# Optimization experiments

Hardware: AMD Instinct MI355X
Metric: run time of the kernel (lower is better)

## Reference

```python
import jax, jax.numpy as jnp
import numpy as np

B = 2; R_PER = 512; R = B * R_PER; RM_PER = 128; RM = B * RM_PER
NUM_CLASSES = 81; C = 256
IMG_H = 800.0; IMG_W = 800.0
SCALES = (0.25, 0.125, 0.0625, 0.03125)  # FPN strides 4,8,16,32
REG_W = (10.0, 10.0, 5.0, 5.0)
LOG_1000_16 = 4.135166556742356  # math.log(1000/16)


def _prep(c, size):
    # torchvision roi_align (aligned=False) coordinate handling
    valid = (c > -1.0) & (c < size)
    c = jnp.clip(c, 0.0, size - 1.0)
    lo = jnp.clip(jnp.floor(c), 0.0, size - 2.0).astype(jnp.int32)
    frac = c - lo.astype(c.dtype)
    return lo, frac, valid


def roi_align(feat, boxes, b_idx, scale, out_size, sr=2):
    # feat [B,C,H,W], boxes [R,4] in image coords, b_idx [R] int
    _, Cn, H, W = feat.shape
    bb = boxes * scale
    x1, y1 = bb[:, 0], bb[:, 1]
    rw = jnp.maximum(bb[:, 2] - x1, 1.0)
    rh = jnp.maximum(bb[:, 3] - y1, 1.0)
    n = out_size * sr
    g = (jnp.arange(n, dtype=feat.dtype) + 0.5) / (sr * out_size)
    ys = y1[:, None] + rh[:, None] * g[None, :]  # [R,n]
    xs = x1[:, None] + rw[:, None] * g[None, :]
    y0, ly, yv = _prep(ys, H)
    x0, lx, xv = _prep(xs, W)
    bi = b_idx[:, None, None]
    yy = y0[:, :, None]; xx = x0[:, None, :]
    f00 = feat[bi, :, yy, xx]          # [R,n,n,C]
    f01 = feat[bi, :, yy, xx + 1]
    f10 = feat[bi, :, yy + 1, xx]
    f11 = feat[bi, :, yy + 1, xx + 1]
    ly_ = ly[:, :, None, None]; lx_ = lx[:, None, :, None]
    v = (f00 * (1 - ly_) * (1 - lx_) + f01 * (1 - ly_) * lx_
         + f10 * ly_ * (1 - lx_) + f11 * ly_ * lx_)
    mask = (yv[:, :, None] & xv[:, None, :]).astype(v.dtype)[..., None]
    v = v * mask
    Rn = boxes.shape[0]
    v = v.reshape(Rn, out_size, sr, out_size, sr, Cn).mean(axis=(2, 4))
    return jnp.transpose(v, (0, 3, 1, 2))  # [R,C,out,out]


def multiscale_roi_align(feats, boxes, b_idx, out_size):
    area = jnp.maximum(boxes[:, 2] - boxes[:, 0], 0.0) * jnp.maximum(boxes[:, 3] - boxes[:, 1], 0.0)
    lvl = jnp.clip(jnp.floor(4.0 + jnp.log2(jnp.sqrt(area) / 224.0 + 1e-6)), 2.0, 5.0).astype(jnp.int32) - 2
    out = 0.0
    for i, (f, s) in enumerate(zip(feats, SCALES)):
        out = out + roi_align(f, boxes, b_idx, s, out_size) * (lvl == i)[:, None, None, None].astype(f.dtype)
    return out


def decode_boxes(deltas, boxes):
    # deltas [R,K,4], boxes [R,4]
    wx, wy, ww, wh = REG_W
    w = boxes[:, 2] - boxes[:, 0]; h = boxes[:, 3] - boxes[:, 1]
    cx = boxes[:, 0] + 0.5 * w; cy = boxes[:, 1] + 0.5 * h
    dx = deltas[..., 0] / wx; dy = deltas[..., 1] / wy
    dw = jnp.minimum(deltas[..., 2] / ww, LOG_1000_16)
    dh = jnp.minimum(deltas[..., 3] / wh, LOG_1000_16)
    pcx = dx * w[:, None] + cx[:, None]; pcy = dy * h[:, None] + cy[:, None]
    pw = jnp.exp(dw) * w[:, None]; ph = jnp.exp(dh) * h[:, None]
    out = jnp.stack([pcx - 0.5 * pw, pcy - 0.5 * ph, pcx + 0.5 * pw, pcy + 0.5 * ph], axis=-1)
    hi = jnp.array([IMG_W, IMG_H, IMG_W, IMG_H], dtype=out.dtype)
    return jnp.clip(out, 0.0, hi)  # process_box clip-to-image


def conv3x3(x, w, b):
    y = jax.lax.conv_general_dilated(x, w, (1, 1), ((1, 1), (1, 1)),
                                     dimension_numbers=('NCHW', 'OIHW', 'NCHW'))
    return jax.nn.relu(y + b[None, :, None, None])


def _forward(feat0, feat1, feat2, feat3, proposals, fc1_w, fc1_b, fc2_w, fc2_b,
             cls_w, cls_b, bbox_w, bbox_b, mconv_w, mconv_b, deconv_w, deconv_b,
             mlogit_w, mlogit_b, batch_idx):
    feats = (feat0, feat1, feat2, feat3)
    # box branch
    bf = multiscale_roi_align(feats, proposals, batch_idx, 7).reshape(R, -1)  # [R, 256*49]
    x = jax.nn.relu(bf @ fc1_w.T + fc1_b)
    x = jax.nn.relu(x @ fc2_w.T + fc2_b)
    scores = jax.nn.softmax(x @ cls_w.T + cls_b, axis=-1)          # [R,81]
    deltas = (x @ bbox_w.T + bbox_b).reshape(R, NUM_CLASSES, 4)
    boxes = decode_boxes(deltas, proposals)                        # [R,81,4]
    # mask branch on top-of-list detections (RM_PER per image), box at argmax fg class
    idx_m = jnp.concatenate([jnp.arange(RM_PER), R_PER + jnp.arange(RM_PER)])
    labels = jnp.argmax(scores[idx_m, 1:], axis=-1) + 1            # [RM]
    mboxes = boxes[idx_m, labels]                                  # [RM,4]
    mf = multiscale_roi_align(feats, mboxes, batch_idx[idx_m], 14)  # [RM,256,14,14]
    for i in range(4):
        mf = conv3x3(mf, mconv_w[i], mconv_b[i])
    # ConvTranspose2d k=2 s=2 (non-overlapping) as einsum, PyTorch IOHW weights
    t = jnp.einsum('bcij,copq->boipjq', mf, deconv_w).reshape(RM, C, 28, 28)
    t = jax.nn.relu(t + deconv_b[None, :, None, None])
    ml = jnp.einsum('bchw,oc->bohw', t, mlogit_w) + mlogit_b[None, :, None, None]
    masks = jax.nn.sigmoid(ml[jnp.arange(RM), labels])             # [RM,28,28]
    return scores, boxes, masks


def setup_inputs() -> dict:
    key = jax.random.key(0)
    ks = jax.random.split(key, 16)
    rn = lambda i, shape, s=1.0: jax.random.normal(ks[i], shape, dtype=jnp.float32) * s
    feat0 = rn(0, (B, C, 200, 200))
    feat1 = rn(1, (B, C, 100, 100))
    feat2 = rn(2, (B, C, 50, 50))
    feat3 = rn(3, (B, C, 25, 25))
    u = jax.random.uniform(ks[4], (R, 4), dtype=jnp.float32)
    x1 = u[:, 0] * (IMG_W - 64.0); y1 = u[:, 1] * (IMG_H - 64.0)
    w = 16.0 + u[:, 2] * 300.0; h = 16.0 + u[:, 3] * 300.0
    proposals = jnp.stack([x1, y1, jnp.minimum(x1 + w, IMG_W), jnp.minimum(y1 + h, IMG_H)], axis=1)
    batch_idx = jnp.repeat(jnp.arange(B, dtype=jnp.int32), R_PER)
    return dict(
        feat0=feat0, feat1=feat1, feat2=feat2, feat3=feat3,
        proposals=proposals,
        fc1_w=rn(5, (1024, C * 49), 0.01), fc1_b=jnp.zeros(1024, jnp.float32),
        fc2_w=rn(6, (1024, 1024), 0.02), fc2_b=jnp.zeros(1024, jnp.float32),
        cls_w=rn(7, (NUM_CLASSES, 1024), 0.02), cls_b=jnp.zeros(NUM_CLASSES, jnp.float32),
        bbox_w=rn(8, (NUM_CLASSES * 4, 1024), 0.01), bbox_b=jnp.zeros(NUM_CLASSES * 4, jnp.float32),
        mconv_w=rn(9, (4, C, C, 3, 3), 0.03), mconv_b=jnp.zeros((4, C), jnp.float32),
        deconv_w=rn(10, (C, C, 2, 2), 0.06), deconv_b=jnp.zeros(C, jnp.float32),
        mlogit_w=rn(11, (NUM_CLASSES, C), 0.06), mlogit_b=jnp.zeros(NUM_CLASSES, jnp.float32),
        batch_idx=batch_idx,
    )


def reference(feat0, feat1, feat2, feat3, proposals, fc1_w, fc1_b, fc2_w, fc2_b,
              cls_w, cls_b, bbox_w, bbox_b, mconv_w, mconv_b, deconv_w, deconv_b,
              mlogit_w, mlogit_b, batch_idx):
    return _forward(feat0, feat1, feat2, feat3, proposals, fc1_w, fc1_b, fc2_w, fc2_b,
                    cls_w, cls_b, bbox_w, bbox_b, mconv_w, mconv_b, deconv_w, deconv_b,
                    mlogit_w, mlogit_b, batch_idx)
```

## Files before the change

### kernel.cpp

```cpp
#include <hip/hip_runtime.h>


#define NUM_CLASSES 81
#define CDIM 256
#define RTOT 1024
#define RMASK 256
#define LOG1000_16 4.135166556742356f

typedef _Float16 half8v __attribute__((ext_vector_type(8)));
typedef _Float16 half4v __attribute__((ext_vector_type(4)));
typedef float    float4v __attribute__((ext_vector_type(4)));
typedef float    float2a4 __attribute__((ext_vector_type(2), aligned(4)));

__device__ __forceinline__ void gload_lds16(const void* g, void* l) {
    __builtin_amdgcn_global_load_lds(
        (const __attribute__((address_space(1))) void*)g,
        (__attribute__((address_space(3))) void*)l, 16, 0, 0);
}

__global__ __launch_bounds__(256) void transpose_nhwc_kernel(
    const float* __restrict__ in, float* __restrict__ out, int H, int W)
{
    __shared__ float tile[64][65];
    int t = threadIdx.x;
    int xl = t & 63, cq = t >> 6;
    int x0 = blockIdx.x * 64;
    int y  = blockIdx.y;
    int b  = blockIdx.z >> 2;
    int c0 = (blockIdx.z & 3) * 64;

    const float* ip = in + (((size_t)(b*CDIM + c0))*H + y)*W + x0;
    if (x0 + xl < W) {
        #pragma unroll
        for (int i = 0; i < 16; ++i) {
            int cl = cq + i*4;
            tile[cl][xl] = ip[(size_t)cl*H*W + xl];
        }
    }
    __syncthreads();
    float* op = out + (((size_t)b*H + y)*W + x0)*CDIM + c0;
    #pragma unroll
    for (int i = 0; i < 16; ++i) {
        int xw = cq + i*4;
        if (x0 + xw < W)
            op[(size_t)xw*CDIM + xl] = tile[xl][xw];
    }
}

__device__ __forceinline__ void axis_taps(
    float start, float ext, int o, float invn, int N,
    float* wgt, int* idx)
{
    #pragma unroll
    for (int s = 0; s < 2; ++s) {
        int i = o*2 + s;
        float g = ((float)i + 0.5f) * invn;
        float c = start + ext*g;
        float mv = ((c > -1.f) && (c < (float)N)) ? 1.f : 0.f;
        float cl = fminf(fmaxf(c, 0.f), (float)(N-1));
        int   i0 = (int)fminf(floorf(cl), (float)(N-2));
        float l  = cl - (float)i0;
        wgt[s*2+0] = (1.f-l)*mv;
        wgt[s*2+1] = l*mv;
        idx[s*2+0] = i0;
        idx[s*2+1] = i0+1;
    }
}

__global__ __launch_bounds__(256) void roi_align7_nhwc_kernel(
    const float* __restrict__ fT0, const float* __restrict__ fT1,
    const float* __restrict__ fT2, const float* __restrict__ fT3,
    const float* __restrict__ props, const int* __restrict__ bidx,
    _Float16* __restrict__ bf_h, _Float16* __restrict__ bf_l)
{
    __shared__ _Float16 lh[256*49];
    __shared__ _Float16 ll[256*49];
    int r = blockIdx.x, t = threadIdx.x;
    int lane = t & 63, wv = t >> 6;

    float x1 = props[r*4+0], y1 = props[r*4+1];
    float x2 = props[r*4+2], y2 = props[r*4+3];
    float area = fmaxf(x2-x1, 0.f) * fmaxf(y2-y1, 0.f);
    float lf = floorf(4.f + log2f(sqrtf(area)/224.f + 1e-6f));
    lf = fminf(fmaxf(lf, 2.f), 5.f);
    int lvl = (int)lf - 2;

    const float* fT; int H, W; float scale;
    if (lvl == 0)      { fT = fT0; H = 200; W = 200; scale = 0.25f; }
    else if (lvl == 1) { fT = fT1; H = 100; W = 100; scale = 0.125f; }
    else if (lvl == 2) { fT = fT2; H = 50;  W = 50;  scale = 0.0625f; }
    else               { fT = fT3; H = 25;  W = 25;  scale = 0.03125f; }
    int b = bidx[r];
    const float* fb = fT + ((size_t)b*H*W)*CDIM + lane*4;

    float x1s = x1*scale, y1s = y1*scale;
    float rw = fmaxf(x2*scale - x1s, 1.f);
    float rh = fmaxf(y2*scale - y1s, 1.f);

    for (int p = wv; p < 49; p += 4) {
        int oy = p / 7, ox = p % 7;
        float uy[4]; int yr[4];
        axis_taps(y1s, rh, oy, 1.f/14.f, H, uy, yr);
        float wx[4]; int xc[4];
        axis_taps(x1s, rw, ox, 1.f/14.f, W, wx, xc);

        float a0 = 0.f, a1 = 0.f, a2 = 0.f, a3 = 0.f;
        #pragma unroll
        for (int a = 0; a < 4; ++a) {
            const float* rowp = fb + (size_t)(yr[a]*W)*CDIM;
            #pragma unroll
            for (int c2 = 0; c2 < 4; ++c2) {
                float w = uy[a]*wx[c2];
                float4v v = *(const float4v*)(rowp + xc[c2]*CDIM);
                a0 += w*v[0]; a1 += w*v[1]; a2 += w*v[2]; a3 += w*v[3];
            }
        }
        float av[4] = {a0, a1, a2, a3};
        #pragma unroll
        for (int e = 0; e < 4; ++e) {
            float vv = av[e]*0.25f;
            _Float16 h = (_Float16)vv;
            int c = lane*4 + e;
            lh[c*49 + p] = h;
            ll[c*49 + p] = (_Float16)((vv - (float)h)*2048.f);
        }
    }
    __syncthreads();
    size_t ob = (size_t)r*12544;
    for (int k = t; k < 12544; k += 256) {
        bf_h[ob + k] = lh[k];
        bf_l[ob + k] = ll[k];
    }
}

__global__ __launch_bounds__(256) void roi_align14_nhwc_kernel(
    const float* __restrict__ fT0, const float* __restrict__ fT1,
    const float* __restrict__ fT2, const float* __restrict__ fT3,
    const float* __restrict__ mboxes, const int* __restrict__ bidx,
    _Float16* __restrict__ outT)
{
    int mi = blockIdx.x, py = blockIdx.y;
    int t = threadIdx.x;
    int lane = t & 63, wv = t >> 6;

    float x1 = mboxes[mi*4+0], y1 = mboxes[mi*4+1];
    float x2 = mboxes[mi*4+2], y2 = mboxes[mi*4+3];
    float area = fmaxf(x2-x1, 0.f) * fmaxf(y2-y1, 0.f);
    float lf = floorf(4.f + log2f(sqrtf(area)/224.f + 1e-6f));
    lf = fminf(fmaxf(lf, 2.f), 5.f);
    int lvl = (int)lf - 2;

    const float* fT; int H, W; float scale;
    if (lvl == 0)      { fT = fT0; H = 200; W = 200; scale = 0.25f; }
    else if (lvl == 1) { fT = fT1; H = 100; W = 100; scale = 0.125f; }
    else if (lvl == 2) { fT = fT2; H = 50;  W = 50;  scale = 0.0625f; }
    else               { fT = fT3; H = 25;  W = 25;  scale = 0.03125f; }
    int ridx = (mi < 128) ? mi : mi + 384;
    int b = bidx[ridx];
    const float* fb = fT + ((size_t)b*H*W)*CDIM + lane*4;

    float x1s = x1*scale, y1s = y1*scale;
    float rw = fmaxf(x2*scale - x1s, 1.f);
    float rh = fmaxf(y2*scale - y1s, 1.f);

    for (int pp = wv; pp < 49; pp += 4) {
        int p = py*49 + pp;
        int oy = p / 14, ox = p % 14;
        float uy[4]; int yr[4];
        axis_taps(y1s, rh, oy, 1.f/28.f, H, uy, yr);
        float wx[4]; int xc[4];
        axis_taps(x1s, rw, ox, 1.f/28.f, W, wx, xc);

        float a0 = 0.f, a1 = 0.f, a2 = 0.f, a3 = 0.f;
        #pragma unroll
        for (int a = 0; a < 4; ++a) {
            const float* rowp = fb + (size_t)(yr[a]*W)*CDIM;
            #pragma unroll
            for (int c2 = 0; c2 < 4; ++c2) {
                float w = uy[a]*wx[c2];
                float4v v = *(const float4v*)(rowp + xc[c2]*CDIM);
                a0 += w*v[0]; a1 += w*v[1]; a2 += w*v[2]; a3 += w*v[3];
            }
        }
        half4v hv;
        hv[0] = (_Float16)(a0*0.25f);
        hv[1] = (_Float16)(a1*0.25f);
        hv[2] = (_Float16)(a2*0.25f);
        hv[3] = (_Float16)(a3*0.25f);
        *(half4v*)(outT + ((size_t)mi*196 + p)*CDIM + lane*4) = hv;
    }
}

__global__ __launch_bounds__(256) void roi_align7_kernel(
    const float* __restrict__ f0, const float* __restrict__ f1,
    const float* __restrict__ f2, const float* __restrict__ f3,
    const float* __restrict__ props, const int* __restrict__ bidx,
    _Float16* __restrict__ bf_h, _Float16* __restrict__ bf_l)
{
    int r  = blockIdx.x;
    int cg = blockIdx.y;
    int t = threadIdx.x;
    if (t >= 196) return;
    int p  = t % 49;
    int cl = t / 49;
    int oy = p / 7, ox = p % 7;

    float x1 = props[r*4+0], y1 = props[r*4+1];
    float x2 = props[r*4+2], y2 = props[r*4+3];
    float area = fmaxf(x2-x1, 0.f) * fmaxf(y2-y1, 0.f);
    float lf = floorf(4.f + log2f(sqrtf(area)/224.f + 1e-6f));
    lf = fminf(fmaxf(lf, 2.f), 5.f);
    int lvl = (int)lf - 2;

    const float* feat; int H, W; float scale;
    if (lvl == 0)      { feat = f0; H = 200; W = 200; scale = 0.25f; }
    else if (lvl == 1) { feat = f1; H = 100; W = 100; scale = 0.125f; }
    else if (lvl == 2) { feat = f2; H = 50;  W = 50;  scale = 0.0625f; }
    else               { feat = f3; H = 25;  W = 25;  scale = 0.03125f; }
    int b = bidx[r];

    float x1s = x1*scale, y1s = y1*scale;
    float rw = fmaxf(x2*scale - x1s, 1.f);
    float rh = fmaxf(y2*scale - y1s, 1.f);

    int   offs[4];
    float w00[4], w01[4], w10[4], w11[4];
    #pragma unroll
    for (int sy = 0; sy < 2; ++sy) {
        int iy = oy*2 + sy;
        float gy = ((float)iy + 0.5f) / 14.f;
        float yc = y1s + rh*gy;
        bool  yv = (yc > -1.f) && (yc < (float)H);
        float ycl = fminf(fmaxf(yc, 0.f), (float)(H-1));
        int   y0  = (int)fminf(floorf(ycl), (float)(H-2));
        float ly  = ycl - (float)y0;
        #pragma unroll
        for (int sx = 0; sx < 2; ++sx) {
            int ix = ox*2 + sx;
            float gx = ((float)ix + 0.5f) / 14.f;
            float xc = x1s + rw*gx;
            bool  xv = (xc > -1.f) && (xc < (float)W);
            float xcl = fminf(fmaxf(xc, 0.f), (float)(W-1));
            int   x0  = (int)fminf(floorf(xcl), (float)(W-2));
            float lx  = xcl - (float)x0;
            float m = (yv && xv) ? 1.f : 0.f;
            int s = sy*2 + sx;
            offs[s] = y0*W + x0;
            w00[s] = (1.f-ly)*(1.f-lx)*m;
            w01[s] = (1.f-ly)*lx*m;
            w10[s] = ly*(1.f-lx)*m;
            w11[s] = ly*lx*m;
        }
    }

    size_t HW = (size_t)H * W;
    #pragma unroll 4
    for (int k = 0; k < 16; ++k) {
        int c = cg*64 + cl + k*4;
        const float* fb = feat + ((size_t)b*CDIM + c) * HW;
        float acc = 0.f;
        #pragma unroll
        for (int s = 0; s < 4; ++s) {
            const float* q = fb + offs[s];
            float2a4 u = *(const float2a4*)q;
            float2a4 v = *(const float2a4*)(q + W);
            acc += w00[s]*u.x + w01[s]*u.y + w10[s]*v.x + w11[s]*v.y;
        }
        float v = acc * 0.25f;
        _Float16 h = (_Float16)v;
        size_t o = (size_t)r*12544 + c*49 + p;
        bf_h[o] = h;
        bf_l[o] = (_Float16)((v - (float)h) * 2048.f);
    }
}

template<int BMODE>
__global__ __launch_bounds__(512, 2) void gemm_fc2(
    const _Float16* __restrict__ Ah, const _Float16* __restrict__ Al,
    const float* __restrict__ B32,
    const _Float16* __restrict__ Bh16, const _Float16* __restrict__ Bl16,
    float* __restrict__ Cp, int K, int KS, int NS)
{
    __shared__ __align__(16) char smem[2*32768];

    int t = threadIdx.x;
    int lane = t & 63, wave = t >> 6;
    int wm = wave >> 2, wn = wave & 3;
    int ln = lane & 15, q = lane >> 4;

    int gx = gridDim.x, gy = gridDim.y;
    int lin = blockIdx.x + gx*(blockIdx.y + gy*blockIdx.z);
    int per = (gx*gy*(int)gridDim.z) >> 3;
    int nl  = (lin & 7)*per + (lin >> 3);
    int bn  = nl % gx;
    int tmp = nl / gx;
    int bm  = tmp % gy;
    int kz  = tmp / gy;

    size_t kbase = (size_t)kz * KS;
    int arow = t >> 2;
    int achk = (lane & 3) ^ ((lane >> 3) & 3);
    const _Float16* Agh = Ah + (size_t)(bm*128 + arow)*K + kbase + achk*8;
    const _Float16* Agl = Al + (size_t)(bm*128 + arow)*K + kbase + achk*8;
    int adst = wave * 512;

    const _Float16 *Bgh = nullptr, *Bgl = nullptr;
    const float *Bg0 = nullptr, *Bg1 = nullptr;
    int bfdst0 = 0, bfdst1 = 0;
    if constexpr (BMODE == 1) {
        Bgh = Bh16 + (size_t)(bn*128 + arow)*K + kbase + achk*8;
        Bgl = Bl16 + (size_t)(bn*128 + arow)*K + kbase + achk*8;
    } else {
        int brow = t >> 3;
        int bchk = (lane & 7) ^ ((lane >> 3) & 7);
        Bg0 = B32 + (size_t)(bn*128 + brow)*K + kbase + bchk*4;
        Bg1 = Bg0 + (size_t)64*K;
        bfdst0 = wave*256;
        bfdst1 = 2048 + wave*256;
    }

    auto AhB = [&](int b){ return (_Float16*)(smem + b*32768); };
    auto AlB = [&](int b){ return (_Float16*)(smem + b*32768 + 8192); };
    auto BhB = [&](int b){ return (_Float16*)(smem + b*32768 + 16384); };
    auto BlB = [&](int b){ return (_Float16*)(smem + b*32768 + 24576); };
    auto BfB = [&](int b){ return (float*)   (smem + b*32768 + 16384); };

    auto dma = [&](int k0, int b) {
        gload_lds16(Agh + k0, AhB(b) + adst);
        gload_lds16(Agl + k0, AlB(b) + adst);
        if constexpr (BMODE == 1) {
            gload_lds16(Bgh + k0, BhB(b) + adst);
            gload_lds16(Bgl + k0, BlB(b) + adst);
        } else {
            gload_lds16(Bg0 + k0, BfB(b) + bfdst0);
            gload_lds16(Bg1 + k0, BfB(b) + bfdst1);
        }
    };

    float4v acc1[4][2], acc2[4][2];
    #pragma unroll
    for (int i = 0; i < 4; ++i)
        #pragma unroll
        for (int j = 0; j < 2; ++j) {
            acc1[i][j] = (float4v){0.f,0.f,0.f,0.f};
            acc2[i][j] = (float4v){0.f,0.f,0.f,0.f};
        }

    int cq = (q ^ ((ln >> 1) & 3)) * 8;

    auto compute = [&](int b) {
        const _Float16* ah = AhB(b);
        const _Float16* al = AlB(b);
        half8v afh[4], afl[4], bfh[2], bfl[2];
        #pragma unroll
        for (int i = 0; i < 4; ++i) {
            int ra = (wm*64 + i*16 + ln)*32 + cq;
            afh[i] = *(const half8v*)&ah[ra];
            afl[i] = *(const half8v*)&al[ra];
        }
        if constexpr (BMODE == 1) {
            const _Float16* bh = BhB(b);
            const _Float16* bl = BlB(b);
            #pragma unroll
            for (int j = 0; j < 2; ++j) {
                int rb = (wn*32 + j*16 + ln)*32 + cq;
                bfh[j] = *(const half8v*)&bh[rb];
                bfl[j] = *(const half8v*)&bl[rb];
            }
        } else {
            const float* bfp = BfB(b);
            #pragma unroll
            for (int j = 0; j < 2; ++j) {
                int row = wn*32 + j*16 + ln;
                int c0 = (q*2)   ^ (row & 7);
                int c1 = (q*2+1) ^ (row & 7);
                float4v f0 = *(const float4v*)&bfp[row*32 + c0*4];
                float4v f1 = *(const float4v*)&bfp[row*32 + c1*4];
                #pragma unroll
                for (int e = 0; e < 4; ++e) {
                    _Float16 h0 = (_Float16)f0[e];
                    bfh[j][e] = h0;
                    bfl[j][e] = (_Float16)((f0[e] - (float)h0) * 2048.f);
                    _Float16 h1 = (_Float16)f1[e];
                    bfh[j][4+e] = h1;
                    bfl[j][4+e] = (_Float16)((f1[e] - (float)h1) * 2048.f);
                }
            }
        }
        #pragma unroll
        for (int i = 0; i < 4; ++i) {
            #pragma unroll
            for (int j = 0; j < 2; ++j) {
                acc1[i][j] = __builtin_amdgcn_mfma_f32_16x16x32_f16(
                    afh[i], bfh[j], acc1[i][j], 0, 0, 0);
                acc2[i][j] = __builtin_amdgcn_mfma_f32_16x16x32_f16(
                    afh[i], bfl[j], acc2[i][j], 0, 0, 0);
                acc2[i][j] = __builtin_amdgcn_mfma_f32_16x16x32_f16(
                    afl[i], bfh[j], acc2[i][j], 0, 0, 0);
            }
        }
    };

    int NT = KS / 32;
    dma(0, 0);
    if (NT > 1) dma(32, 1);

    for (int tt = 0; tt < NT; ++tt) {
        if (tt < NT-1) asm volatile("s_waitcnt vmcnt(4)" ::: "memory");
        else           asm volatile("s_waitcnt vmcnt(0)" ::: "memory");
        __builtin_amdgcn_s_barrier();
        asm volatile("" ::: "memory");
        compute(tt & 1);
        asm volatile("" ::: "memory");
        __builtin_amdgcn_s_barrier();
        if (tt + 2 < NT) dma((tt+2)*32, tt & 1);
    }

    float* Cpz = Cp + (size_t)kz*1024*NS;
    #pragma unroll
    for (int i = 0; i < 4; ++i) {
        #pragma unroll
        for (int j = 0; j < 2; ++j) {
            int col = bn*128 + wn*32 + j*16 + ln;
            #pragma unroll
            for (int reg = 0; reg < 4; ++reg) {
                int row = bm*128 + wm*64 + i*16 + q*4 + reg;
                Cpz[(size_t)row*NS + col] =
                    acc1[i][j][reg] + acc2[i][j][reg] * (1.f/2048.f);
            }
        }
    }
}

__global__ __launch_bounds__(256) void fc_reduce_kernel(
    const float* __restrict__ Cp, const float* __restrict__ bias,
    float* __restrict__ out, _Float16* __restrict__ outh,
    _Float16* __restrict__ outl, int nparts, int ns4, int do_relu)
{
    int i = blockIdx.x*256 + threadIdx.x;
    const float4* p = (const float4*)Cp;
    int pstride = 1024*ns4;
    float sx = 0.f, sy = 0.f, sz = 0.f, sw = 0.f;
    for (int j = 0; j < nparts; ++j) {
        float4 s = p[i + j*pstride];
        sx += s.x; sy += s.y; sz += s.z; sw += s.w;
    }
    float4 b4 = ((const float4*)bias)[i & (ns4-1)];
    float4 v;
    v.x = sx + b4.x; v.y = sy + b4.y; v.z = sz + b4.z; v.w = sw + b4.w;
    if (do_relu) {
        v.x = fmaxf(v.x, 0.f); v.y = fmaxf(v.y, 0.f);
        v.z = fmaxf(v.z, 0.f); v.w = fmaxf(v.w, 0.f);
    }
    if (out) ((float4*)out)[i] = v;
    if (outh) {
        float vv[4] = {v.x, v.y, v.z, v.w};
        half4v hh, hl;
        #pragma unroll
        for (int c2 = 0; c2 < 4; ++c2) {
            _Float16 h = (_Float16)vv[c2];
            hh[c2] = h;
            hl[c2] = (_Float16)((vv[c2] - (float)h) * 2048.f);
        }
        ((half4v*)outh)[i] = hh;
        ((half4v*)outl)[i] = hl;
    }
}

__global__ __launch_bounds__(256) void repack_split_kernel(
    const float* __restrict__ w, _Float16* __restrict__ h,
    _Float16* __restrict__ l)
{
    int i = blockIdx.x*256 + threadIdx.x;
    float4 v = ((const float4*)w)[i];
    float vv[4] = {v.x, v.y, v.z, v.w};
    half4v hh, hl;
    #pragma unroll
    for (int c2 = 0; c2 < 4; ++c2) {
        _Float16 hj = (_Float16)vv[c2];
        hh[c2] = hj;
        hl[c2] = (_Float16)((vv[c2] - (float)hj) * 2048.f);
    }
    ((half4v*)h)[i] = hh;
    ((half4v*)l)[i] = hl;
}

__global__ __launch_bounds__(256) void repack_head_kernel(
    const float* __restrict__ cls_w, const float* __restrict__ cls_b,
    const float* __restrict__ bbox_w, const float* __restrict__ bbox_b,
    _Float16* __restrict__ Wcat_h, _Float16* __restrict__ Wcat_l,
    float* __restrict__ bcat)
{
    int i = blockIdx.x*256 + threadIdx.x;
    int row = i >> 10, col = i & 1023;
    float v = 0.f;
    if (row < 81) v = cls_w[row*1024 + col];
    else if (row < 405) v = bbox_w[(row-81)*1024 + col];
    _Float16 h = (_Float16)v;
    Wcat_h[i] = h;
    Wcat_l[i] = (_Float16)((v - (float)h) * 2048.f);
    if (i < 512) {
        float bv = 0.f;
        if (i < 81) bv = cls_b[i];
        else if (i < 405) bv = bbox_b[i-81];
        bcat[i] = bv;
    }
}

__global__ __launch_bounds__(128) void heads_finish_kernel(
    const float* __restrict__ L, const float* __restrict__ props,
    float* __restrict__ scores, float* __restrict__ boxes,
    int* __restrict__ labels, float* __restrict__ mboxes)
{
    __shared__ float lg[NUM_CLASSES];
    __shared__ float red[2];
    __shared__ int slab;
    int r = blockIdx.x, t = threadIdx.x;
    const float* Lr = L + (size_t)r*512;
    if (t < NUM_CLASSES) lg[t] = Lr[t];
    __syncthreads();
    if (t == 0) {
        float mx = lg[0];
        for (int j = 1; j < NUM_CLASSES; ++j) mx = fmaxf(mx, lg[j]);
        red[0] = mx;
    }
    __syncthreads();
    float mx = red[0];
    if (t < NUM_CLASSES) lg[t] = expf(lg[t] - mx);
    __syncthreads();
    if (t == 0) {
        float s = 0.f;
        int best = 1; float bv = lg[1];
        for (int j = 0; j < NUM_CLASSES; ++j) {
            s += lg[j];
            if (j >= 1 && lg[j] > bv) { bv = lg[j]; best = j; }
        }
        red[1] = 1.f/s;
        slab = best;
    }
    __syncthreads();
    if (t < NUM_CLASSES) scores[(size_t)r*NUM_CLASSES + t] = lg[t]*red[1];

    bool sel = (r < 128) || (r >= 512 && r < 640);
    int mi = (r < 128) ? r : r - 384;
    if (t == 0 && sel) labels[mi] = slab;

    if (t < NUM_CLASSES) {
        float px1 = props[r*4+0], py1 = props[r*4+1];
        float px2 = props[r*4+2], py2 = props[r*4+3];
        float pw = px2 - px1, ph = py2 - py1;
        float cx = px1 + 0.5f*pw, cy = py1 + 0.5f*ph;
        const float* dl = Lr + 81 + t*4;
        float d0 = dl[0] * 0.1f;
        float d1 = dl[1] * 0.1f;
        float d2 = fminf(dl[2] * 0.2f, LOG1000_16);
        float d3 = fminf(dl[3] * 0.2f, LOG1000_16);
        float pcx = d0*pw + cx, pcy = d1*ph + cy;
        float qw = expf(d2)*pw, qh = expf(d3)*ph;
        float b0 = fminf(fmaxf(pcx - 0.5f*qw, 0.f), 800.f);
        float b1 = fminf(fmaxf(pcy - 0.5f*qh, 0.f), 800.f);
        float b2 = fminf(fmaxf(pcx + 0.5f*qw, 0.f), 800.f);
        float b3 = fminf(fmaxf(pcy + 0.5f*qh, 0.f), 800.f);
        size_t ob = ((size_t)r*NUM_CLASSES + t)*4;
        boxes[ob+0] = b0; boxes[ob+1] = b1; boxes[ob+2] = b2; boxes[ob+3] = b3;
        if (sel && t == slab) {
            mboxes[mi*4+0] = b0; mboxes[mi*4+1] = b1;
            mboxes[mi*4+2] = b2; mboxes[mi*4+3] = b3;
        }
    }
}

__global__ __launch_bounds__(256) void roi_align14_kernel(
    const float* __restrict__ f0, const float* __restrict__ f1,
    const float* __restrict__ f2, const float* __restrict__ f3,
    const float* __restrict__ mboxes, const int* __restrict__ bidx,
    _Float16* __restrict__ outT)
{
    int mi = blockIdx.x;
    int cg = blockIdx.y;
    int t = threadIdx.x;
    if (t >= 196) return;
    int oy = t / 14, ox = t % 14;

    float x1 = mboxes[mi*4+0], y1 = mboxes[mi*4+1];
    float x2 = mboxes[mi*4+2], y2 = mboxes[mi*4+3];
    float area = fmaxf(x2-x1, 0.f) * fmaxf(y2-y1, 0.f);
    float lf = floorf(4.f + log2f(sqrtf(area)/224.f + 1e-6f));
    lf = fminf(fmaxf(lf, 2.f), 5.f);
    int lvl = (int)lf - 2;

    const float* feat; int H, W; float scale;
    if (lvl == 0)      { feat = f0; H = 200; W = 200; scale = 0.25f; }
    else if (lvl == 1) { feat = f1; H = 100; W = 100; scale = 0.125f; }
    else if (lvl == 2) { feat = f2; H = 50;  W = 50;  scale = 0.0625f; }
    else               { feat = f3; H = 25;  W = 25;  scale = 0.03125f; }
    int ridx = (mi < 128) ? mi : mi + 384;
    int b = bidx[ridx];

    float x1s = x1*scale, y1s = y1*scale;
    float rw = fmaxf(x2*scale - x1s, 1.f);
    float rh = fmaxf(y2*scale - y1s, 1.f);

    int   offs[4];
    float w00[4], w01[4], w10[4], w11[4];
    #pragma unroll
    for (int sy = 0; sy < 2; ++sy) {
        int iy = oy*2 + sy;
        float gy = ((float)iy + 0.5f) / 28.f;
        float yc = y1s + rh*gy;
        bool  yv = (yc > -1.f) && (yc < (float)H);
        float ycl = fminf(fmaxf(yc, 0.f), (float)(H-1));
        int   y0  = (int)fminf(floorf(ycl), (float)(H-2));
        float ly  = ycl - (float)y0;
        #pragma unroll
        for (int sx = 0; sx < 2; ++sx) {
            int ix = ox*2 + sx;
            float gx = ((float)ix + 0.5f) / 28.f;
            float xc = x1s + rw*gx;
            bool  xv = (xc > -1.f) && (xc < (float)W);
            float xcl = fminf(fmaxf(xc, 0.f), (float)(W-1));
            int   x0  = (int)fminf(floorf(xcl), (float)(W-2));
            float lx  = xcl - (float)x0;
            float m = (yv && xv) ? 1.f : 0.f;
            int s = sy*2 + sx;
            offs[s] = y0*W + x0;
            w00[s] = (1.f-ly)*(1.f-lx)*m;
            w01[s] = (1.f-ly)*lx*m;
            w10[s] = ly*(1.f-lx)*m;
            w11[s] = ly*lx*m;
        }
    }

    size_t HW = (size_t)H * W;
    _Float16* orow = outT + ((size_t)mi*196 + t)*CDIM + cg*32;
    const float* fbase = feat + ((size_t)b*CDIM + cg*32) * HW;
    #pragma unroll
    for (int c8 = 0; c8 < 32; c8 += 8) {
        half8v hv;
        #pragma unroll
        for (int cc = 0; cc < 8; ++cc) {
            const float* fb = fbase + (size_t)(c8+cc) * HW;
            float acc = 0.f;
            #pragma unroll
            for (int s = 0; s < 4; ++s) {
                const float* q = fb + offs[s];
                float2a4 u = *(const float2a4*)q;
                float2a4 v = *(const float2a4*)(q + W);
                acc += w00[s]*u.x + w01[s]*u.y + w10[s]*v.x + w11[s]*v.y;
            }
            hv[cc] = (_Float16)(acc * 0.25f);
        }
        *(half8v*)(orow + c8) = hv;
    }
}

__global__ __launch_bounds__(256) void repack_wts_kernel(
    const float* __restrict__ w, _Float16* __restrict__ Wr)
{
    int i = blockIdx.x*256 + threadIdx.x;
    int ci = i & 255;
    int rest = i >> 8;
    int co = rest & 255;
    int rest2 = rest >> 8;
    int tap = rest2 % 9;
    int l = rest2 / 9;
    Wr[i] = (_Float16)w[(((size_t)(l*256 + co)*256 + ci)*9) + tap];
}

__global__ __launch_bounds__(256) void repack_dw_kernel(
    const float* __restrict__ dw, _Float16* __restrict__ Wd)
{
    int i = blockIdx.x*256 + threadIdx.x;
    int n = i >> 8, k = i & 255;
    Wd[i] = (_Float16)dw[(size_t)k*1024 + n];
}

#define PSTR 40

__global__ __launch_bounds__(256, 2) void conv3x3_mfma_kernel(
    const _Float16* __restrict__ inT, const _Float16* __restrict__ Wr,
    const float* __restrict__ bias, _Float16* __restrict__ outT, int layer)
{
    __shared__ _Float16 lin[256*PSTR];

    int t = threadIdx.x;
    int lane = t & 63;
    int wave = t >> 6;
    int ln = lane & 15;
    int q  = lane >> 4;
    int q8 = q*8;
    int r  = blockIdx.x >> 1;
    int bc = blockIdx.x & 1;
    int co_w = bc*128 + wave*32;

    const _Float16* WrL = Wr + (size_t)layer*9*256*256;
    const _Float16* inR = inT + (size_t)r*196*256;

    for (int i = t; i < 256*PSTR; i += 256) lin[i] = (_Float16)0.f;

    float4v acc[13][2];
    #pragma unroll
    for (int nt = 0; nt < 13; ++nt) {
        acc[nt][0] = (float4v){0.f,0.f,0.f,0.f};
        acc[nt][1] = (float4v){0.f,0.f,0.f,0.f};
    }

    for (int ci0 = 0; ci0 < 256; ci0 += 32) {
        __syncthreads();
        for (int idx = t; idx < 784; idx += 256) {
            int p = idx >> 2, g = idx & 3;
            float4 v = *(const float4*)(inR + (size_t)p*256 + ci0 + g*8);
            int row = (p*37450) >> 19;
            int col = p - row*14;
            *(float4*)&lin[((row+1)*16 + (col+1))*PSTR + g*8] = v;
        }
        __syncthreads();

        half8v aw[9][2];
        #pragma unroll
        for (int tap = 0; tap < 9; ++tap) {
            #pragma unroll
            for (int u = 0; u < 2; ++u)
                aw[tap][u] = *(const half8v*)(
                    WrL + ((size_t)tap*256 + co_w + u*16 + ln)*256 + ci0 + q8);
        }

        #pragma unroll
        for (int nt = 0; nt < 13; ++nt) {
            int n = nt*16 + ln;
            int row = (n*37450) >> 19;
            int col = n - row*14;
            int pb = (n < 196) ? (row*16 + col) : 0;
            const _Float16* bp = &lin[pb*PSTR + q8];
            #pragma unroll
            for (int ky = 0; ky < 3; ++ky) {
                #pragma unroll
                for (int kx = 0; kx < 3; ++kx) {
                    half8v bv = *(const half8v*)(bp + (ky*16 + kx)*PSTR);
                    acc[nt][0] = __builtin_amdgcn_mfma_f32_16x16x32_f16(
                        aw[ky*3+kx][0], bv, acc[nt][0], 0, 0, 0);
                    acc[nt][1] = __builtin_amdgcn_mfma_f32_16x16x32_f16(
                        aw[ky*3+kx][1], bv, acc[nt][1], 0, 0, 0);
                }
            }
        }
    }

    #pragma unroll
    for (int u = 0; u < 2; ++u) {
        float4 bi = *(const float4*)&bias[layer*256 + co_w + u*16 + q*4];
        float bia[4] = {bi.x, bi.y, bi.z, bi.w};
        #pragma unroll
        for (int nt = 0; nt < 13; ++nt) {
            int n = nt*16 + ln;
            if (n < 196) {
                half4v hv;
                #pragma unroll
                for (int i = 0; i < 4; ++i)
                    hv[i] = (_Float16)fmaxf(acc[nt][u][i] + bia[i], 0.f);
                *(half4v*)(outT + ((size_t)r*196 + n)*256 + co_w + u*16 + q*4) = hv;
            }
        }
    }
}

#define DSTR 264

template<int NMT>
__device__ __forceinline__ void deconv_pass(
    const _Float16* actL, const _Float16* __restrict__ Wd,
    const float* __restrict__ db, const float* __restrict__ mlw,
    int lab, float (*sred)[4], int wv, int ln, int q, int px0)
{
    float P[NMT][4];
    #pragma unroll
    for (int mt = 0; mt < NMT; ++mt)
        #pragma unroll
        for (int r2 = 0; r2 < 4; ++r2) P[mt][r2] = 0.f;

    for (int c = 0; c < 8; ++c) {
        int n0 = wv*256 + c*32;
        float4v acc[NMT][2];
        #pragma unroll
        for (int mt = 0; mt < NMT; ++mt) {
            acc[mt][0] = (float4v){0.f,0.f,0.f,0.f};
            acc[mt][1] = (float4v){0.f,0.f,0.f,0.f};
        }
        #pragma unroll
        for (int k = 0; k < 8; ++k) {
            const _Float16* wp = Wd + ((size_t)(n0 + ln))*256 + k*32 + q*8;
            half8v b0 = *(const half8v*)wp;
            half8v b1 = *(const half8v*)(wp + 16*256);
            #pragma unroll
            for (int mt = 0; mt < NMT; ++mt) {
                half8v a = *(const half8v*)&actL[(mt*16 + ln)*DSTR + k*32 + q*8];
                acc[mt][0] = __builtin_amdgcn_mfma_f32_16x16x32_f16(
                    a, b0, acc[mt][0], 0, 0, 0);
                acc[mt][1] = __builtin_amdgcn_mfma_f32_16x16x32_f16(
                    a, b1, acc[mt][1], 0, 0, 0);
            }
        }
        #pragma unroll
        for (int j = 0; j < 2; ++j) {
            int n = n0 + j*16 + ln;
            int o = n >> 2;
            float bo = db[o];
            float wl = mlw[lab*256 + o];
            #pragma unroll
            for (int mt = 0; mt < NMT; ++mt)
                #pragma unroll
                for (int r2 = 0; r2 < 4; ++r2)
                    P[mt][r2] += fmaxf(acc[mt][j][r2] + bo, 0.f) * wl;
        }
    }
    #pragma unroll
    for (int mt = 0; mt < NMT; ++mt)
        #pragma unroll
        for (int r2 = 0; r2 < 4; ++r2) {
            float v = P[mt][r2];
            v += __shfl_xor(v, 4);
            v += __shfl_xor(v, 8);
            int px = px0 + mt*16 + q*4 + r2;
            if (ln < 4 && px < 196) atomicAdd(&sred[px][ln], v);
        }
}

__global__ __launch_bounds__(256, 1) void deconv_mask_mfma_kernel(
    const _Float16* __restrict__ mfT, const _Float16* __restrict__ Wd,
    const float* __restrict__ db, const float* __restrict__ mlw,
    const float* __restrict__ mlb, const int* __restrict__ labels,
    float* __restrict__ masks)
{
    __shared__ _Float16 act[112*DSTR];
    __shared__ float sred[196][4];
    int t = threadIdx.x;
    int lane = t & 63, wv = t >> 6, ln = lane & 15, q = lane >> 4;
    int mi = blockIdx.x;
    int lab = labels[mi];

    for (int i = t; i < 784; i += 256) ((float*)sred)[i] = 0.f;

    for (int idx = t; idx < 112*32; idx += 256) {
        int px = idx >> 5, g = idx & 31;
        *(float4*)&act[px*DSTR + g*8] =
            *(const float4*)(mfT + ((size_t)mi*196 + px)*256 + g*8);
    }
    __syncthreads();
    deconv_pass<7>(act, Wd, db, mlw, lab, sred, wv, ln, q, 0);
    __syncthreads();

    for (int idx = t; idx < 84*32; idx += 256) {
        int px = idx >> 5, g = idx & 31;
        *(float4*)&act[px*DSTR + g*8] =
            *(const float4*)(mfT + ((size_t)mi*196 + 112 + px)*256 + g*8);
    }
    __syncthreads();
    deconv_pass<6>(act, Wd, db, mlw, lab, sred, wv, ln, q, 112);
    __syncthreads();

    if (t < 196) {
        float bl = mlb[lab];
        int i2 = t / 14, j2 = t % 14;
        #pragma unroll
        for (int pq = 0; pq < 4; ++pq) {
            float s = sred[t][pq] + bl;
            int h = 2*i2 + (pq >> 1), w2 = 2*j2 + (pq & 1);
            masks[(size_t)mi*784 + h*28 + w2] = 1.f/(1.f + expf(-s));
        }
    }
}

extern "C" void kernel_launch(void* const* d_in, const int* in_sizes, int n_in,
                              void* d_out, int out_size, void* d_ws, size_t ws_size,
                              hipStream_t stream) {
    const float* f0      = (const float*)d_in[0];
    const float* f1      = (const float*)d_in[1];
    const float* f2      = (const float*)d_in[2];
    const float* f3      = (const float*)d_in[3];
    const float* props   = (const float*)d_in[4];
    const float* fc1_w   = (const float*)d_in[5];
    const float* fc1_b   = (const float*)d_in[6];
    const float* fc2_w   = (const float*)d_in[7];
    const float* fc2_b   = (const float*)d_in[8];
    const float* cls_w   = (const float*)d_in[9];
    const float* cls_b   = (const float*)d_in[10];
    const float* bbox_w  = (const float*)d_in[11];
    const float* bbox_b  = (const float*)d_in[12];
    const float* mconv_w = (const float*)d_in[13];
    const float* mconv_b = (const float*)d_in[14];
    const float* dconv_w = (const float*)d_in[15];
    const float* dconv_b = (const float*)d_in[16];
    const float* mlog_w  = (const float*)d_in[17];
    const float* mlog_b  = (const float*)d_in[18];
    const int*   bidx    = (const int*)d_in[19];

    char* wsb = (char*)d_ws;
    _Float16* bf_h = (_Float16*)wsb;
    _Float16* bf_l = (_Float16*)(wsb + 25690112);
    _Float16* fc2h = (_Float16*)wsb;
    _Float16* fc2l = (_Float16*)(wsb + 2097152);
    _Float16* bufA = (_Float16*)wsb;
    _Float16* bufB = (_Float16*)(wsb + 25690112);
    _Float16* x1h  = (_Float16*)(wsb + 51380224);
    _Float16* x1l  = (_Float16*)(wsb + 53477376);
    _Float16* x2h  = (_Float16*)(wsb + 55574528);
    _Float16* x2l  = (_Float16*)(wsb + 57671680);
    int*      labels = (int*)(wsb + 59768832);
    float*    mboxes = (float*)(wsb + 59772928);
    float*    Cp     = (float*)(wsb + 59781120);
    _Float16* Wr     = (_Float16*)(wsb + 59781120);
    _Float16* Wd     = (_Float16*)(wsb + 64499712);
    _Float16* Wcat_h = (_Float16*)(wsb + 76558336);
    _Float16* Wcat_l = (_Float16*)(wsb + 77606912);
    float*    bcat   = (float*)(wsb + 78655488);
    float*    Lh     = (float*)(wsb + 78659584);
    float*    fT0    = (float*)(wsb + 80756736);
    float*    fT1    = (float*)(wsb + 162676736);
    float*    fT2    = (float*)(wsb + 183156736);
    float*    fT3    = (float*)(wsb + 188276736);
    bool nhwc = (ws_size >= 189556736ull);
    _Float16* fc1wh  = (_Float16*)(wsb + 189556736);
    _Float16* fc1wl  = (_Float16*)(wsb + 215246848);
    bool fc1split = (ws_size >= 240936960ull);

    float* scores = (float*)d_out;
    float* boxes  = scores + RTOT*NUM_CLASSES;
    float* masks  = boxes + RTOT*NUM_CLASSES*4;

    if (nhwc) {
        transpose_nhwc_kernel<<<dim3(4, 200, 8), 256, 0, stream>>>(f0, fT0, 200, 200);
        transpose_nhwc_kernel<<<dim3(2, 100, 8), 256, 0, stream>>>(f1, fT1, 100, 100);
        transpose_nhwc_kernel<<<dim3(1,  50, 8), 256, 0, stream>>>(f2, fT2,  50,  50);
        transpose_nhwc_kernel<<<dim3(1,  25, 8), 256, 0, stream>>>(f3, fT3,  25,  25);
        roi_align7_nhwc_kernel<<<RTOT, 256, 0, stream>>>(
            fT0, fT1, fT2, fT3, props, bidx, bf_h, bf_l);
    } else {
        roi_align7_kernel<<<dim3(RTOT, 4), 256, 0, stream>>>(
            f0, f1, f2, f3, props, bidx, bf_h, bf_l);
    }

    repack_head_kernel<<<2048, 256, 0, stream>>>(cls_w, cls_b, bbox_w, bbox_b,
                                                 Wcat_h, Wcat_l, bcat);

    if (fc1split) {
        repack_split_kernel<<<12544, 256, 0, stream>>>(fc1_w, fc1wh, fc1wl);
        gemm_fc2<1><<<dim3(8, 8, 4), 512, 0, stream>>>(
            bf_h, bf_l, nullptr, fc1wh, fc1wl, Cp, 12544, 3136, 1024);
    } else {
        gemm_fc2<0><<<dim3(8, 8, 4), 512, 0, stream>>>(
            bf_h, bf_l, fc1_w, nullptr, nullptr, Cp, 12544, 3136, 1024);
    }
    fc_reduce_kernel<<<1024, 256, 0, stream>>>(Cp, fc1_b, nullptr, x1h, x1l,
                                               4, 256, 1);

    repack_split_kernel<<<1024, 256, 0, stream>>>(fc2_w, fc2h, fc2l);

    gemm_fc2<1><<<dim3(8, 8, 4), 512, 0, stream>>>(
        x1h, x1l, nullptr, fc2h, fc2l, Cp, 1024, 256, 1024);
    fc_reduce_kernel<<<1024, 256, 0, stream>>>(Cp, fc2_b, nullptr, x2h, x2l,
                                               4, 256, 1);

    gemm_fc2<1><<<dim3(4, 8, 8), 512, 0, stream>>>(
        x2h, x2l, nullptr, Wcat_h, Wcat_l, Cp, 1024, 128, 512);
    fc_reduce_kernel<<<512, 256, 0, stream>>>(Cp, bcat, Lh, nullptr, nullptr,
                                              8, 128, 0);

    heads_finish_kernel<<<RTOT, 128, 0, stream>>>(Lh, props, scores, boxes,
                                                  labels, mboxes);

    repack_wts_kernel<<<4*9*256, 256, 0, stream>>>(mconv_w, Wr);
    repack_dw_kernel<<<1024, 256, 0, stream>>>(dconv_w, Wd);

    if (nhwc) {
        roi_align14_nhwc_kernel<<<dim3(RMASK, 4), 256, 0, stream>>>(
            fT0, fT1, fT2, fT3, mboxes, bidx, bufA);
    } else {
        roi_align14_kernel<<<dim3(RMASK, 8), 256, 0, stream>>>(
            f0, f1, f2, f3, mboxes, bidx, bufA);
    }

    conv3x3_mfma_kernel<<<RMASK*2, 256, 0, stream>>>(bufA, Wr, mconv_b, bufB, 0);
    conv3x3_mfma_kernel<<<RMASK*2, 256, 0, stream>>>(bufB, Wr, mconv_b, bufA, 1);
    conv3x3_mfma_kernel<<<RMASK*2, 256, 0, stream>>>(bufA, Wr, mconv_b, bufB, 2);
    conv3x3_mfma_kernel<<<RMASK*2, 256, 0, stream>>>(bufB, Wr, mconv_b, bufA, 3);

    deconv_mask_mfma_kernel<<<RMASK, 256, 0, stream>>>(bufA, Wd, dconv_b, mlog_w,
                                                       mlog_b, labels, masks);
}
```

Baseline: 849.7 us.

## Widen conv3x3 block to all output channels and split FC GEMMs over more K-chunks

The mask conv kernel now has each block cover all 256 output channels of one ROI (64 per wave), so the input tile is staged into shared memory once per ROI instead of twice. This halves the grid to 256 blocks and doubles the accumulators per thread, with launch bounds lowered to one block per SM. Separately, the fc1 and fc2 GEMMs use split-K of 8 instead of 4 into a new workspace partial buffer, giving more blocks for parallelism at the cost of a larger reduction. The new GEMM path is used only when the workspace is large enough.

```diff
diff --git a/kernel.cpp b/kernel.cpp
--- a/kernel.cpp
+++ b/kernel.cpp
@@ -677,7 +677,7 @@
 
 #define PSTR 40
 
-__global__ __launch_bounds__(256, 2) void conv3x3_mfma_kernel(
+__global__ __launch_bounds__(256, 1) void conv3x3_mfma_kernel(
     const _Float16* __restrict__ inT, const _Float16* __restrict__ Wr,
     const float* __restrict__ bias, _Float16* __restrict__ outT, int layer)
 {
@@ -689,21 +689,29 @@
     int ln = lane & 15;
     int q  = lane >> 4;
     int q8 = q*8;
-    int r  = blockIdx.x >> 1;
-    int bc = blockIdx.x & 1;
-    int co_w = bc*128 + wave*32;
+    int r  = blockIdx.x;
+    int co_w = wave*64;
 
     const _Float16* WrL = Wr + (size_t)layer*9*256*256;
     const _Float16* inR = inT + (size_t)r*196*256;
 
     for (int i = t; i < 256*PSTR; i += 256) lin[i] = (_Float16)0.f;
 
-    float4v acc[13][2];
+    int pb[13];
     #pragma unroll
     for (int nt = 0; nt < 13; ++nt) {
-        acc[nt][0] = (float4v){0.f,0.f,0.f,0.f};
-        acc[nt][1] = (float4v){0.f,0.f,0.f,0.f};
-    }
+        int n = nt*16 + ln;
+        int row = (n*37450) >> 19;
+        int col = n - row*14;
+        pb[nt] = (n < 196) ? (row*16 + col) : 0;
+    }
+
+    float4v acc[13][4];
+    #pragma unroll
+    for (int nt = 0; nt < 13; ++nt)
+        #pragma unroll
+        for (int u = 0; u < 4; ++u)
+            acc[nt][u] = (float4v){0.f,0.f,0.f,0.f};
 
     for (int ci0 = 0; ci0 < 256; ci0 += 32) {
         __syncthreads();
@@ -716,38 +724,34 @@
         }
         __syncthreads();
 
-        half8v aw[9][2];
         #pragma unroll
         for (int tap = 0; tap < 9; ++tap) {
+            const int toff = ((tap/3)*16 + (tap%3)) * PSTR;
+            half8v aw0 = *(const half8v*)(
+                WrL + ((size_t)tap*256 + co_w +  0 + ln)*256 + ci0 + q8);
+            half8v aw1 = *(const half8v*)(
+                WrL + ((size_t)tap*256 + co_w + 16 + ln)*256 + ci0 + q8);
+            half8v aw2 = *(const half8v*)(
+                WrL + ((size_t)tap*256 + co_w + 32 + ln)*256 + ci0 + q8);
+            half8v aw3 = *(const half8v*)(
+                WrL + ((size_t)tap*256 + co_w + 48 + ln)*256 + ci0 + q8);
             #pragma unroll
-            for (int u = 0; u < 2; ++u)
-                aw[tap][u] = *(const half8v*)(
-                    WrL + ((size_t)tap*256 + co_w + u*16 + ln)*256 + ci0 + q8);
-        }
-
-        #pragma unroll
-        for (int nt = 0; nt < 13; ++nt) {
-            int n = nt*16 + ln;
-            int row = (n*37450) >> 19;
-            int col = n - row*14;
-            int pb = (n < 196) ? (row*16 + col) : 0;
-            const _Float16* bp = &lin[pb*PSTR + q8];
-            #pragma unroll
-            for (int ky = 0; ky < 3; ++ky) {
-                #pragma unroll
-                for (int kx = 0; kx < 3; ++kx) {
-                    half8v bv = *(const half8v*)(bp + (ky*16 + kx)*PSTR);
-                    acc[nt][0] = __builtin_amdgcn_mfma_f32_16x16x32_f16(
-                        aw[ky*3+kx][0], bv, acc[nt][0], 0, 0, 0);
-                    acc[nt][1] = __builtin_amdgcn_mfma_f32_16x16x32_f16(
-                        aw[ky*3+kx][1], bv, acc[nt][1], 0, 0, 0);
-                }
+            for (int nt = 0; nt < 13; ++nt) {
+                half8v bv = *(const half8v*)&lin[pb[nt]*PSTR + toff + q8];
+                acc[nt][0] = __builtin_amdgcn_mfma_f32_16x16x32_f16(
+                    aw0, bv, acc[nt][0], 0, 0, 0);
+                acc[nt][1] = __builtin_amdgcn_mfma_f32_16x16x32_f16(
+                    aw1, bv, acc[nt][1], 0, 0, 0);
+                acc[nt][2] = __builtin_amdgcn_mfma_f32_16x16x32_f16(
+                    aw2, bv, acc[nt][2], 0, 0, 0);
+                acc[nt][3] = __builtin_amdgcn_mfma_f32_16x16x32_f16(
+                    aw3, bv, acc[nt][3], 0, 0, 0);
             }
         }
     }
 
     #pragma unroll
-    for (int u = 0; u < 2; ++u) {
+    for (int u = 0; u < 4; ++u) {
         float4 bi = *(const float4*)&bias[layer*256 + co_w + u*16 + q*4];
         float bia[4] = {bi.x, bi.y, bi.z, bi.w};
         #pragma unroll
@@ -922,6 +926,8 @@
     _Float16* fc1wh  = (_Float16*)(wsb + 189556736);
     _Float16* fc1wl  = (_Float16*)(wsb + 215246848);
     bool fc1split = (ws_size >= 240936960ull);
+    float*    Cp8    = (float*)(wsb + 240936960);
+    bool cp8ok = (ws_size >= 274491392ull);
 
     float* scores = (float*)d_out;
     float* boxes  = scores + RTOT*NUM_CLASSES;
@@ -944,21 +950,37 @@
 
     if (fc1split) {
         repack_split_kernel<<<12544, 256, 0, stream>>>(fc1_w, fc1wh, fc1wl);
-        gemm_fc2<1><<<dim3(8, 8, 4), 512, 0, stream>>>(
-            bf_h, bf_l, nullptr, fc1wh, fc1wl, Cp, 12544, 3136, 1024);
+        if (cp8ok) {
+            gemm_fc2<1><<<dim3(8, 8, 8), 512, 0, stream>>>(
+                bf_h, bf_l, nullptr, fc1wh, fc1wl, Cp8, 12544, 1568, 1024);
+            fc_reduce_kernel<<<1024, 256, 0, stream>>>(Cp8, fc1_b, nullptr,
+                                                       x1h, x1l, 8, 256, 1);
+        } else {
+            gemm_fc2<1><<<dim3(8, 8, 4), 512, 0, stream>>>(
+                bf_h, bf_l, nullptr, fc1wh, fc1wl, Cp, 12544, 3136, 1024);
+            fc_reduce_kernel<<<1024, 256, 0, stream>>>(Cp, fc1_b, nullptr,
+                                                       x1h, x1l, 4, 256, 1);
+        }
     } else {
         gemm_fc2<0><<<dim3(8, 8, 4), 512, 0, stream>>>(
             bf_h, bf_l, fc1_w, nullptr, nullptr, Cp, 12544, 3136, 1024);
-    }
-    fc_reduce_kernel<<<1024, 256, 0, stream>>>(Cp, fc1_b, nullptr, x1h, x1l,
-                                               4, 256, 1);
+        fc_reduce_kernel<<<1024, 256, 0, stream>>>(Cp, fc1_b, nullptr,
+                                                   x1h, x1l, 4, 256, 1);
+    }
 
     repack_split_kernel<<<1024, 256, 0, stream>>>(fc2_w, fc2h, fc2l);
 
-    gemm_fc2<1><<<dim3(8, 8, 4), 512, 0, stream>>>(
-        x1h, x1l, nullptr, fc2h, fc2l, Cp, 1024, 256, 1024);
-    fc_reduce_kernel<<<1024, 256, 0, stream>>>(Cp, fc2_b, nullptr, x2h, x2l,
-                                               4, 256, 1);
+    if (cp8ok) {
+        gemm_fc2<1><<<dim3(8, 8, 8), 512, 0, stream>>>(
+            x1h, x1l, nullptr, fc2h, fc2l, Cp8, 1024, 128, 1024);
+        fc_reduce_kernel<<<1024, 256, 0, stream>>>(Cp8, fc2_b, nullptr,
+                                                   x2h, x2l, 8, 256, 1);
+    } else {
+        gemm_fc2<1><<<dim3(8, 8, 4), 512, 0, stream>>>(
+            x1h, x1l, nullptr, fc2h, fc2l, Cp, 1024, 256, 1024);
+        fc_reduce_kernel<<<1024, 256, 0, stream>>>(Cp, fc2_b, nullptr,
+                                                   x2h, x2l, 4, 256, 1);
+    }
 
     gemm_fc2<1><<<dim3(4, 8, 8), 512, 0, stream>>>(
         x2h, x2l, nullptr, Wcat_h, Wcat_l, Cp, 1024, 128, 512);
@@ -979,10 +1001,10 @@
             f0, f1, f2, f3, mboxes, bidx, bufA);
     }
 
-    conv3x3_mfma_kernel<<<RMASK*2, 256, 0, stream>>>(bufA, Wr, mconv_b, bufB, 0);
-    conv3x3_mfma_kernel<<<RMASK*2, 256, 0, stream>>>(bufB, Wr, mconv_b, bufA, 1);
-    conv3x3_mfma_kernel<<<RMASK*2, 256, 0, stream>>>(bufA, Wr, mconv_b, bufB, 2);
-    conv3x3_mfma_kernel<<<RMASK*2, 256, 0, stream>>>(bufB, Wr, mconv_b, bufA, 3);
+    conv3x3_mfma_kernel<<<RMASK, 256, 0, stream>>>(bufA, Wr, mconv_b, bufB, 0);
+    conv3x3_mfma_kernel<<<RMASK, 256, 0, stream>>>(bufB, Wr, mconv_b, bufA, 1);
+    conv3x3_mfma_kernel<<<RMASK, 256, 0, stream>>>(bufA, Wr, mconv_b, bufB, 2);
+    conv3x3_mfma_kernel<<<RMASK, 256, 0, stream>>>(bufB, Wr, mconv_b, bufA, 3);
 
     deconv_mask_mfma_kernel<<<RMASK, 256, 0, stream>>>(bufA, Wd, dconv_b, mlog_w,
                                                        mlog_b, labels, masks);
```

Result: slower. 1.009 ms (+18.8%).
